# Kernel optimization log

Hardware: AMD Instinct MI355X
Metric: run time of the kernel (lower is better)

Reference implementation:

```python
import jax, jax.numpy as jnp
import numpy as np

B, T, U, V, H = 64, 800, 100, 80, 512
KA, KO = 10, 20
ATT_MULT = 0.05


def setup_inputs() -> dict:
    key = jax.random.key(0)
    ks = jax.random.split(key, 16)
    s = 0.05
    inp = {
        'chars': jax.random.randint(ks[0], (B, U), 0, V, dtype=jnp.int32),
        'chars_mask': jnp.ones((B, U), jnp.float32),
        'strokes': jax.random.normal(ks[1], (B, T, 3), jnp.float32),
        'strokes_mask': jnp.ones((B, T), jnp.float32),
        # lstm_0: LSTMCell(3+V -> H), PyTorch gate order i,f,g,o; biases fused
        'W_ih0': jax.random.normal(ks[2], (4 * H, 3 + V), jnp.float32) * s,
        'W_hh0': jax.random.normal(ks[3], (4 * H, H), jnp.float32) * s,
        'b0': jnp.zeros((4 * H,), jnp.float32),
        # attention linear: H -> 3*KA
        'W_att': jax.random.normal(ks[4], (3 * KA, H), jnp.float32) * s,
        'b_att': jnp.zeros((3 * KA,), jnp.float32),
        # lstm_1: (3+V+H -> H)
        'W_ih1': jax.random.normal(ks[5], (4 * H, 3 + V + H), jnp.float32) * s,
        'W_hh1': jax.random.normal(ks[6], (4 * H, H), jnp.float32) * s,
        'b1': jnp.zeros((4 * H,), jnp.float32),
        # lstm_2: (3+V+H -> H)
        'W_ih2': jax.random.normal(ks[7], (4 * H, 3 + V + H), jnp.float32) * s,
        'W_hh2': jax.random.normal(ks[8], (4 * H, H), jnp.float32) * s,
        'b2': jnp.zeros((4 * H,), jnp.float32),
        # fc: 3H -> 6*KO + 1
        'W_fc': jax.random.normal(ks[9], (6 * KO + 1, 3 * H), jnp.float32) * s,
        'b_fc': jnp.zeros((6 * KO + 1,), jnp.float32),
    }
    return inp


def _lstm_step(h, c, x, W_ih, W_hh, b):
    gates = x @ W_ih.T + h @ W_hh.T + b
    i, f, g, o = jnp.split(gates, 4, axis=-1)
    c = jax.nn.sigmoid(f) * c + jax.nn.sigmoid(i) * jnp.tanh(g)
    h = jax.nn.sigmoid(o) * jnp.tanh(c)
    return h, c


def _lstm_layer(x_btd, W_ih, W_hh, b):
    # x_btd: [B, T, D] -> [B, T, H]
    def step(carry, x_t):
        h, c = carry
        h, c = _lstm_step(h, c, x_t, W_ih, W_hh, b)
        return (h, c), h
    h0 = jnp.zeros((x_btd.shape[0], H), x_btd.dtype)
    c0 = jnp.zeros_like(h0)
    _, hs = jax.lax.scan(step, (h0, c0), jnp.swapaxes(x_btd, 0, 1))
    return jnp.swapaxes(hs, 0, 1)


def _forward(chars, chars_mask, strokes, strokes_mask,
             W_ih0, W_hh0, b0, W_att, b_att,
             W_ih1, W_hh1, b1, W_ih2, W_hh2, b2, W_fc, b_fc):
    ctx = jax.nn.one_hot(chars, V, dtype=jnp.float32) * chars_mask[..., None]  # [B,U,V]
    u = jnp.arange(U, dtype=jnp.float32)  # [U]

    def step(carry, x_t):
        h0, c0, w_t, k_t = carry
        h0, c0 = _lstm_step(h0, c0, jnp.concatenate([x_t, w_t], -1), W_ih0, W_hh0, b0)
        abk = jnp.exp(h0 @ W_att.T + b_att)  # [B, 3*KA]
        alpha, beta, kappa = jnp.split(abk, 3, axis=-1)  # each [B, KA]
        kappa = kappa * ATT_MULT + k_t
        # phi: [B, U]
        phi = jnp.sum(alpha[:, None, :] * jnp.exp(-beta[:, None, :] * (kappa[:, None, :] - u[None, :, None]) ** 2), axis=-1)
        phi = phi * chars_mask
        w_t = jnp.einsum('bu,buv->bv', phi, ctx)
        return (h0, c0, w_t, kappa), (h0, w_t)

    init = (jnp.zeros((B, H)), jnp.zeros((B, H)), jnp.zeros((B, V)), jnp.zeros((B, KA)))
    _, (h0_seq, w_seq) = jax.lax.scan(step, init, jnp.swapaxes(strokes, 0, 1))
    lstm0_out = jnp.swapaxes(h0_seq, 0, 1)      # [B,T,H]
    att_out = jnp.swapaxes(w_seq, 0, 1)         # [B,T,V]

    lstm1_out = _lstm_layer(jnp.concatenate([strokes, att_out, lstm0_out], -1), W_ih1, W_hh1, b1)
    lstm2_out = _lstm_layer(jnp.concatenate([strokes, att_out, lstm1_out], -1), W_ih2, W_hh2, b2)

    last = jnp.concatenate([lstm0_out, lstm1_out, lstm2_out], -1) @ W_fc.T + b_fc  # [B,T,6*KO+1]
    mu, log_sigma, pi, rho, eos = jnp.split(last, [2 * KO, 4 * KO, 5 * KO, 6 * KO], axis=-1)
    rho = jnp.tanh(rho)
    log_pi = jax.nn.log_softmax(pi, axis=-1)
    eos = jax.nn.sigmoid(-eos)
    # packed output: [log_pi | mu | log_sigma | rho | eos] -> [B,T,6*KO+1]
    return jnp.concatenate([log_pi, mu, log_sigma, rho, eos], axis=-1)


def reference(chars, chars_mask, strokes, strokes_mask,
              W_ih0, W_hh0, b0, W_att, b_att,
              W_ih1, W_hh1, b1, W_ih2, W_hh2, b2, W_fc, b_fc):
    return _forward(chars, chars_mask, strokes, strokes_mask,
                    W_ih0, W_hh0, b0, W_att, b_att,
                    W_ih1, W_hh1, b1, W_ih2, W_hh2, b2, W_fc, b_fc)
```

## Files before the change

### kernel.cpp

```cpp
#include <hip/hip_runtime.h>


#define TT   800
#define NOUT 121
#define NEG  (-1073741824)
typedef unsigned long long u64;
typedef unsigned int u32;
typedef __attribute__((ext_vector_type(8))) short short8v;
typedef __attribute__((ext_vector_type(4))) float float4v;

#define RSLOT   65536
#define RWSLOT  12288
#define OFF_SEQ 0
#define OFF_R0  16384
#define OFF_R1  (OFF_R0 + 16 * RSLOT)
#define OFF_R2  (OFF_R1 + 16 * RSLOT)
#define OFF_RW  (OFF_R2 + 16 * RSLOT)
#define OFF_WATT (OFF_RW + 16 * RWSLOT)
#define OFF_OV  (OFF_WATT + 65536)
#define ABLK    36864
#define OFF_WA1 (OFF_OV + 801 * 4096)
#define OFF_WA2 (OFF_WA1 + 256 * ABLK)
#define OFF_WFC (OFF_WA2 + 128 * ABLK)
#define OFF_END (OFF_WFC + 8 * 48 * 1024)

#define MFMA_B16(a, b, c) __builtin_amdgcn_mfma_f32_16x16x32_bf16(a, b, c, 0, 0, 0)

__device__ __forceinline__ float sigmf(float x) { return 1.f / (1.f + __expf(-x)); }
__device__ __forceinline__ float tanhf_(float x) { return 1.f - 2.f / (1.f + __expf(2.f * x)); }
__device__ __forceinline__ unsigned short f2bf(float x) {
    u32 u = __float_as_uint(x);
    return (unsigned short)((u + 0x7FFFu + ((u >> 16) & 1u)) >> 16);
}
__device__ __forceinline__ float bf2f(u32 s) { return __uint_as_float(s << 16); }

__device__ __forceinline__ u64 cl64(const u64* p) {
    return __hip_atomic_load(p, __ATOMIC_RELAXED, __HIP_MEMORY_SCOPE_AGENT);
}
__device__ __forceinline__ u32 cl32(const u32* p) {
    return __hip_atomic_load(p, __ATOMIC_RELAXED, __HIP_MEMORY_SCOPE_AGENT);
}
__device__ __forceinline__ void cs32(u32* p, u32 v) {
    __hip_atomic_store(p, v, __ATOMIC_RELAXED, __HIP_MEMORY_SCOPE_AGENT);
}
__device__ __forceinline__ void cs64(u64* p, u64 v) {
    __hip_atomic_store(p, v, __ATOMIC_RELAXED, __HIP_MEMORY_SCOPE_AGENT);
}

__global__ void prep_zero(u32* ws32) {
    int n = (OFF_WATT - OFF_SEQ) / 4;
    for (int i = blockIdx.x * blockDim.x + threadIdx.x; i < n; i += gridDim.x * blockDim.x) {
        u32 v = 0u;
        if (i < 4096 && (i & 31) == 0) {
            int f = i >> 5;
            if (f >= 104 && f < 128) v = 0x7FFFFFFFu;
        }
        ws32[i] = v;
    }
}
__global__ void prep_ov(const float* __restrict__ strokes, short* __restrict__ dst) {
    int n = 801 * 2048;
    for (int idx = blockIdx.x * blockDim.x + threadIdx.x; idx < n; idx += gridDim.x * blockDim.x) {
        int s = idx >> 11, rem = idx & 2047;
        int t = rem >> 9, lane = (rem >> 3) & 63, j = rem & 7;
        int k = 1088 + (lane >> 4) * 8 + j;
        int b = t * 16 + (lane & 15);
        short v = 0;
        int tt = -1, d = 0;
        if (k >= 1104 && k <= 1106)      { tt = s - 1; d = k - 1104; }
        else if (k >= 1107 && k <= 1109) { tt = s;     d = k - 1107; }
        if (tt >= 0 && tt < TT) v = (short)f2bf(strokes[((size_t)b * TT + tt) * 3 + d]);
        dst[idx] = v;
    }
}
__global__ void prep_watt(const float* __restrict__ W_att, short* __restrict__ dst) {
    int n = 2 * 2 * 16 * 512;
    for (int idx = blockIdx.x * blockDim.x + threadIdx.x; idx < n; idx += gridDim.x * blockDim.x) {
        int part = idx >> 14;
        int mt = (idx >> 13) & 1;
        int c = (idx >> 9) & 15;
        int lane = (idx >> 3) & 63, j = idx & 7;
        int a = mt * 16 + (lane & 15);
        int k = c * 32 + ((lane >> 4) << 3) + j;
        float v = (a < 30) ? W_att[a * 512 + k] : 0.f;
        unsigned short h = f2bf(v);
        if (part) { float r = v - bf2f(h); h = f2bf(r); }
        dst[idx] = (short)h;
    }
}
__global__ void prep_wa1(const float* __restrict__ Wih0, const float* __restrict__ Whh0,
                         const float* __restrict__ Wih1, const float* __restrict__ Whh1,
                         short* __restrict__ dst) {
    int n = 256 * 36 * 512;
    for (int idx = blockIdx.x * blockDim.x + threadIdx.x; idx < n; idx += gridDim.x * blockDim.x) {
        int blk = idx / 18432, rem = idx % 18432;
        int c = rem >> 9, r2 = rem & 511, lane = r2 >> 3, j = r2 & 7;
        int m = lane & 15, q = lane >> 4;
        int k = c * 32 + q * 8 + j;
        int gate = m & 3, hloc = m >> 2;
        float v = 0.f;
        if (blk < 128) {
            int grow = gate * 512 + blk * 4 + hloc;
            if (k >= 512 && k < 1024)       v = Whh0[(size_t)grow * 512 + (k - 512)];
            else if (k >= 1024 && k < 1104) v = Wih0[(size_t)grow * 83 + 3 + (k - 1024)];
            else if (k >= 1107 && k < 1110) v = Wih0[(size_t)grow * 83 + (k - 1107)];
        } else {
            int grow = gate * 512 + (blk - 128) * 4 + hloc;
            if (k < 512)        v = Whh1[(size_t)grow * 512 + k];
            else if (k < 1024)  v = Wih1[(size_t)grow * 595 + 83 + (k - 512)];
            else if (k < 1104)  v = Wih1[(size_t)grow * 595 + 3 + (k - 1024)];
            else if (k < 1107)  v = Wih1[(size_t)grow * 595 + (k - 1104)];
        }
        dst[idx] = (short)f2bf(v);
    }
}
__global__ void prep_wa2(const float* __restrict__ Wih2, const float* __restrict__ Whh2,
                         short* __restrict__ dst) {
    int n = 128 * 36 * 512;
    for (int idx = blockIdx.x * blockDim.x + threadIdx.x; idx < n; idx += gridDim.x * blockDim.x) {
        int blk = idx / 18432, rem = idx % 18432;
        int c = rem >> 9, r2 = rem & 511, lane = r2 >> 3, j = r2 & 7;
        int m = lane & 15, q = lane >> 4;
        int k = c * 32 + q * 8 + j;
        int grow = (m & 3) * 512 + blk * 4 + (m >> 2);
        float v = 0.f;
        if (k < 512)        v = Whh2[(size_t)grow * 512 + k];
        else if (k < 1024)  v = Wih2[(size_t)grow * 595 + 83 + (k - 512)];
        else if (k < 1104)  v = Wih2[(size_t)grow * 595 + 3 + (k - 1024)];
        else if (k < 1107)  v = Wih2[(size_t)grow * 595 + (k - 1104)];
        dst[idx] = (short)f2bf(v);
    }
}
__global__ void prep_wfc(const float* __restrict__ W_fc, short* __restrict__ dst) {
    int n = 8 * 48 * 512;
    for (int idx = blockIdx.x * blockDim.x + threadIdx.x; idx < n; idx += gridDim.x * blockDim.x) {
        int mt = idx / 24576, rem = idx % 24576;
        int c = rem >> 9, r2 = rem & 511, lane = r2 >> 3, j = r2 & 7;
        int o = mt * 16 + (lane & 15);
        int k = c * 32 + (lane >> 4) * 8 + j;
        float v = (o < NOUT) ? W_fc[(size_t)o * 1536 + k] : 0.f;
        dst[idx] = (short)f2bf(v);
    }
}

__device__ __forceinline__ void waitf2(u32* SEQ, int i1, int t1, int i2, int t2, int wv) {
    if (wv == 0) {
        int sl = 0;
        while (1) {
            int v1 = (int)cl32(SEQ + i1 * 32);
            int v2 = (int)cl32(SEQ + i2 * 32);
            if (__all((v1 >= t1) & (v2 >= t2))) break;
            if (sl < 7) ++sl;
            switch (sl) {
                case 3: __builtin_amdgcn_s_sleep(1); break;
                case 4: __builtin_amdgcn_s_sleep(2); break;
                case 5: __builtin_amdgcn_s_sleep(4); break;
                case 6: __builtin_amdgcn_s_sleep(8); break;
                case 7: __builtin_amdgcn_s_sleep(16); break;
                default: break;
            }
        }
    }
    __syncthreads();
}
__device__ __forceinline__ void waitf1(u32* SEQ, int i1, int t1, int wv) {
    if (wv == 0) {
        int sl = 0;
        while (1) {
            int v1 = (int)cl32(SEQ + i1 * 32);
            if (__all(v1 >= t1)) break;
            if (sl < 7) ++sl;
            switch (sl) {
                case 3: __builtin_amdgcn_s_sleep(1); break;
                case 4: __builtin_amdgcn_s_sleep(2); break;
                case 5: __builtin_amdgcn_s_sleep(4); break;
                case 6: __builtin_amdgcn_s_sleep(8); break;
                case 7: __builtin_amdgcn_s_sleep(16); break;
                default: break;
            }
        }
    }
    __syncthreads();
}
__device__ __forceinline__ void publish(u32* SEQ, int idx, int val) {
    asm volatile("s_waitcnt vmcnt(0)" ::: "memory");
    __syncthreads();
    if (threadIdx.x == 0) cs32(SEQ + idx * 32, (u32)val);
}

__device__ __forceinline__ void store_h(char* slot, int nb, int mt, int nt,
                                        int q, int nn, u32 hb) {
    u32 g1 = (u32)__shfl((int)hb, nn + 16, 64);
    u32 g2 = (u32)__shfl((int)hb, nn + 32, 64);
    u32 g3 = (u32)__shfl((int)hb, nn + 48, 64);
    if (q == 0) {
        int k0 = nb * 16 + mt * 4;
        int ck = k0 >> 5, qq = (k0 >> 3) & 3, j0 = k0 & 7;
        u64 pk = (u64)(hb & 0xFFFFu) | ((u64)(g1 & 0xFFFFu) << 16)
               | ((u64)(g2 & 0xFFFFu) << 32) | ((u64)(g3 & 0xFFFFu) << 48);
        u64* dst = (u64*)(slot + ((((ck * 4 + nt) * 64 + qq * 16 + nn) * 8 + j0) * 2));
        cs64(dst, pk);
    }
}

__device__ __forceinline__ float4v gemm_run(const short* __restrict__ Ab,
                                            const short* __restrict__ pB,
                                            int c0, int cN, float4v acc) {
    short8v a0 = *(const short8v*)(Ab + (size_t)(c0 + 0) * 512);
    short8v a1 = *(const short8v*)(Ab + (size_t)(c0 + 1) * 512);
    short8v a2 = *(const short8v*)(Ab + (size_t)(c0 + 2) * 512);
    short8v a3 = *(const short8v*)(Ab + (size_t)(c0 + 3) * 512);
    short8v a4 = *(const short8v*)(Ab + (size_t)(c0 + 4) * 512);
    short8v a5 = *(const short8v*)(Ab + (size_t)(c0 + 5) * 512);
    short8v a6 = *(const short8v*)(Ab + (size_t)(c0 + 6) * 512);
    short8v a7 = *(const short8v*)(Ab + (size_t)(c0 + 7) * 512);
    int c = c0;
    short8v bv;
#pragma unroll 1
    for (; c + 8 < cN; c += 8) {
        bv = *(const short8v*)(pB + (size_t)(c + 0) * 2048);
        acc = MFMA_B16(a0, bv, acc);
        if (c + 8 < cN)  a0 = *(const short8v*)(Ab + (size_t)(c + 8) * 512);
        bv = *(const short8v*)(pB + (size_t)(c + 1) * 2048);
        acc = MFMA_B16(a1, bv, acc);
        if (c + 9 < cN)  a1 = *(const short8v*)(Ab + (size_t)(c + 9) * 512);
        bv = *(const short8v*)(pB + (size_t)(c + 2) * 2048);
        acc = MFMA_B16(a2, bv, acc);
        if (c + 10 < cN) a2 = *(const short8v*)(Ab + (size_t)(c + 10) * 512);
        bv = *(const short8v*)(pB + (size_t)(c + 3) * 2048);
        acc = MFMA_B16(a3, bv, acc);
        if (c + 11 < cN) a3 = *(const short8v*)(Ab + (size_t)(c + 11) * 512);
        bv = *(const short8v*)(pB + (size_t)(c + 4) * 2048);
        acc = MFMA_B16(a4, bv, acc);
        if (c + 12 < cN) a4 = *(const short8v*)(Ab + (size_t)(c + 12) * 512);
        bv = *(const short8v*)(pB + (size_t)(c + 5) * 2048);
        acc = MFMA_B16(a5, bv, acc);
        if (c + 13 < cN) a5 = *(const short8v*)(Ab + (size_t)(c + 13) * 512);
        bv = *(const short8v*)(pB + (size_t)(c + 6) * 2048);
        acc = MFMA_B16(a6, bv, acc);
        if (c + 14 < cN) a6 = *(const short8v*)(Ab + (size_t)(c + 14) * 512);
        bv = *(const short8v*)(pB + (size_t)(c + 7) * 2048);
        acc = MFMA_B16(a7, bv, acc);
        if (c + 15 < cN) a7 = *(const short8v*)(Ab + (size_t)(c + 15) * 512);
    }
    int r = cN - c;
    bv = *(const short8v*)(pB + (size_t)(c + 0) * 2048);
    acc = MFMA_B16(a0, bv, acc);
    if (r > 1) { bv = *(const short8v*)(pB + (size_t)(c + 1) * 2048); acc = MFMA_B16(a1, bv, acc); }
    if (r > 2) { bv = *(const short8v*)(pB + (size_t)(c + 2) * 2048); acc = MFMA_B16(a2, bv, acc); }
    if (r > 3) { bv = *(const short8v*)(pB + (size_t)(c + 3) * 2048); acc = MFMA_B16(a3, bv, acc); }
    if (r > 4) { bv = *(const short8v*)(pB + (size_t)(c + 4) * 2048); acc = MFMA_B16(a4, bv, acc); }
    if (r > 5) { bv = *(const short8v*)(pB + (size_t)(c + 5) * 2048); acc = MFMA_B16(a5, bv, acc); }
    if (r > 6) { bv = *(const short8v*)(pB + (size_t)(c + 6) * 2048); acc = MFMA_B16(a6, bv, acc); }
    if (r > 7) { bv = *(const short8v*)(pB + (size_t)(c + 7) * 2048); acc = MFMA_B16(a7, bv, acc); }
    return acc;
}

__global__ void __launch_bounds__(1024, 4)
hand_pipeline(const int* __restrict__ chars, const float* __restrict__ chars_mask,
              const float* __restrict__ b_att,
              const float* __restrict__ b0, const float* __restrict__ b1,
              const float* __restrict__ b2, const float* __restrict__ b_fc,
              float* ws, float* __restrict__ out) {
    __shared__ short panel[36 * 4 * 64 * 8];
    char* wsB = (char*)ws;
    u32* SEQ = (u32*)(wsB + OFF_SEQ);
    u64* pan8 = (u64*)panel;
    const int tid = threadIdx.x;
    const int blk = blockIdx.x;
    const int lid = tid & 63;
    const int wv  = __builtin_amdgcn_readfirstlane(tid >> 6);
    const int q   = lid >> 4, nn = lid & 15;
    const int mt  = wv >> 2, nt = wv & 3;
    const int role = blk >> 5;
    const int nb   = blk & 31;

    float* ABK  = (float*)panel;
    float* KAP  = ABK + 2048;
    float* WCTX = KAP + 640;
    unsigned char* CH8 = (unsigned char*)(WCTX + 5184);
    float* M2   = (float*)(CH8 + 6400);
    float* BATT = M2 + 6400;

    for (int i = tid; i < 18432; i += 1024) pan8[i] = 0ull;
    __syncthreads();

    float biasr[4] = {0.f, 0.f, 0.f, 0.f};
    if (role < 3) {
        const float* bp = role == 0 ? b0 : role == 1 ? b1 : b2;
        int hg = nb * 16 + mt * 4 + q;
#pragma unroll
        for (int r = 0; r < 4; ++r) biasr[r] = bp[r * 512 + hg];
    }
    if (role == 0) {
        for (int i = tid; i < 6400; i += 1024) {
            int u2 = i >> 6, b = i & 63;
            CH8[i] = (unsigned char)chars[b * 100 + u2];
            float m = chars_mask[b * 100 + u2];
            M2[i] = m * m;
        }
        if (tid < 640) KAP[tid] = 0.f;
        if (tid < 32) BATT[tid] = (tid < 30) ? b_att[tid] : 0.f;
    }
    __syncthreads();

    const short* WA1 = (const short*)(wsB + OFF_WA1);
    const short* WA2 = (const short*)(wsB + OFF_WA2);
    float cst = 0.f;

    if (role == 0) {
        const short* Ab = WA1 + (size_t)(nb * 4 + mt) * 18432 + lid * 8;
        const short* pB = panel + (size_t)(nt * 64 + lid) * 8;
        for (int s = 0; s <= TT; ++s) {
            if ((s & 7) == 0) waitf2(SEQ, 32 + lid, s - 8, 96 + (lid & 7), s - 8, wv);
            {
                const u64* sO = (const u64*)(wsB + OFF_OV + (size_t)s * 4096);
                if (tid < 512) pan8[17408 + tid] = sO[tid];
#pragma unroll
                for (int it = 0; it < 6; ++it) {
                    int i = tid + it * 1024;
                    if (i < 5184) WCTX[i] = 0.f;
                }
            }
            waitf1(SEQ, lid & 31, s, wv);
            {
                const u64* sB = (const u64*)(wsB + OFF_R0 + (size_t)((s - 1) & 15) * RSLOT);
                u64 tb[8];
#pragma unroll
                for (int it = 0; it < 8; ++it) tb[it] = cl64(sB + tid + it * 1024);
#pragma unroll
                for (int it = 0; it < 8; ++it) pan8[8192 + tid + it * 1024] = tb[it];
            }
            __syncthreads();
            const bool actA = (s >= 1);
            float4v acc = {0.f, 0.f, 0.f, 0.f};
            if (wv >= 8) {
                if (s < TT) acc = gemm_run(Ab, pB, 16, 32, acc);
            } else if (actA) {
                const int mta = mt & 1;
                const short* Ah = (const short*)(wsB + OFF_WATT) + (size_t)mta * 8192 + lid * 8;
                const short* Al = Ah + 16384;
                const short* pBA = panel + (size_t)((64 + nt) * 64 + lid) * 8;
                float4v aacc = {0.f, 0.f, 0.f, 0.f};
#pragma unroll 4
                for (int c = 0; c < 16; ++c) {
                    short8v bv = *(const short8v*)(pBA + (size_t)c * 2048);
                    aacc = MFMA_B16(*(const short8v*)(Ah + (size_t)c * 512), bv, aacc);
                    aacc = MFMA_B16(*(const short8v*)(Al + (size_t)c * 512), bv, aacc);
                }
#pragma unroll
                for (int r = 0; r < 4; ++r) {
                    int a = mta * 16 + q * 4 + r;
                    if (a < 30) ABK[a * 64 + nt * 16 + nn] = __expf(aacc[r] + BATT[a]);
                }
            }
            __syncthreads();
            if (actA) {
                const int b = tid & 63;
                float al[10], be[10], kp[10];
#pragma unroll
                for (int ka = 0; ka < 10; ++ka) {
                    al[ka] = ABK[ka * 64 + b];
                    be[ka] = ABK[(10 + ka) * 64 + b];
                    kp[ka] = KAP[ka * 64 + b] + 0.05f * ABK[(20 + ka) * 64 + b];
                }
                for (int i = tid; i < 6400; i += 1024) {
                    float fu = (float)(i >> 6);
                    float ph = 0.f;
#pragma unroll
                    for (int ka = 0; ka < 10; ++ka) {
                        float d = kp[ka] - fu;
                        ph = fmaf(al[ka], __expf(-be[ka] * d * d), ph);
                    }
                    float m2 = M2[i];
                    if (m2 != 0.f) atomicAdd(&WCTX[b * 81 + CH8[i]], ph * m2);
                }
            }
            __syncthreads();
            if (wv < 8) {
                if (s < TT) acc = gemm_run(Ab, pB, 16, 32, acc);
            } else if (actA) {
                const int st = tid - 512;
#pragma unroll
                for (int ii = 0; ii < 2; ++ii) {
                    int i = st + ii * 512;
                    if (i < 640) KAP[i] += 0.05f * ABK[(20 + (i >> 6)) * 64 + (i & 63)];
                }
                for (int idx = st; idx < 6144; idx += 512) {
                    int c = idx >> 11, rem = idx & 2047;
                    int nt2 = rem >> 9, l = (rem >> 3) & 63, j = rem & 7;
                    int k = 1024 + c * 32 + ((l >> 4) << 3) + j;
                    if (k < 1104) {
                        int b = nt2 * 16 + (l & 15);
                        panel[(size_t)(((32 + c) * 4 + nt2) * 64 + l) * 8 + j] =
                            (short)f2bf(WCTX[b * 81 + (k - 1024)]);
                    }
                }
                if (st < 80) {
                    int bsel = st / 40, p = st - bsel * 40;
                    int bb = nb * 2 + bsel;
                    int k = 1024 + p * 2;
                    int lc = (k - 1024) >> 5, qq = (k >> 3) & 3, j = k & 7;
                    char* slot = wsB + OFF_RW + (size_t)((s - 1) & 15) * RWSLOT;
                    u32* dst = (u32*)(slot +
                        ((((lc * 4 + (bb >> 4)) * 64 + qq * 16 + (bb & 15)) * 8 + j) * 2));
                    cs32(dst, (u32)f2bf(WCTX[bb * 81 + 2 * p]) |
                              ((u32)f2bf(WCTX[bb * 81 + 2 * p + 1]) << 16));
                }
            }
            __syncthreads();
            if (s < TT) {
#pragma unroll
                for (int c = 32; c < 35; ++c) {
                    short8v av = *(const short8v*)(Ab + (size_t)c * 512);
                    short8v bv = *(const short8v*)(pB + (size_t)c * 2048);
                    acc = MFMA_B16(av, bv, acc);
                }
                float gi = acc[0] + biasr[0], gf = acc[1] + biasr[1];
                float gg = acc[2] + biasr[2], go = acc[3] + biasr[3];
                cst = sigmf(gf) * cst + sigmf(gi) * tanhf_(gg);
                float h = sigmf(go) * tanhf_(cst);
                store_h(wsB + OFF_R0 + (size_t)(s & 15) * RSLOT, nb, mt, nt, q, nn, f2bf(h));
            }
            publish(SEQ, blk, s + 1);
        }
    } else if (role < 3) {
        const short* Ab = (role == 1 ? WA1 + (size_t)(128 + nb * 4 + mt) * 18432
                                     : WA2 + (size_t)(nb * 4 + mt) * 18432) + lid * 8;
        const short* pB = panel + (size_t)(nt * 64 + lid) * 8;
        for (int t = 0; t < TT; ++t) {
            if ((t & 7) == 0) {
                if (role == 1) waitf2(SEQ, 64 + (lid & 31), t - 8, 96 + (lid & 7), t - 8, wv);
                else           waitf1(SEQ, 96 + (lid & 7), t - 8, wv);
            }
            if (role == 1) waitf1(SEQ, 32 + (lid & 31), t, wv);
            else           waitf1(SEQ, 64 + (lid & 31), t, wv);
            const u64* sA = (const u64*)(wsB + (role == 1 ? OFF_R1 : OFF_R2) +
                                         (size_t)((t - 1) & 15) * RSLOT);
            u64 ta[8];
#pragma unroll
            for (int it = 0; it < 8; ++it) ta[it] = cl64(sA + tid + it * 1024);
            if (role == 1) waitf1(SEQ, lid & 31, t + 2, wv);
            else           waitf1(SEQ, lid, (lid < 32) ? t + 2 : t + 1, wv);
            {
                const u64* sB = (role == 1)
                    ? (const u64*)(wsB + OFF_R0 + (size_t)(t & 15) * RSLOT)
                    : (const u64*)(wsB + OFF_R1 + (size_t)(t & 15) * RSLOT);
                const u64* sW = (const u64*)(wsB + OFF_RW + (size_t)(t & 15) * RWSLOT);
                const u64* sO = (const u64*)(wsB + OFF_OV + (size_t)(t + 1) * 4096);
                u64 tb[8];
#pragma unroll
                for (int it = 0; it < 8; ++it) tb[it] = cl64(sB + tid + it * 1024);
                u64 tw = cl64(sW + tid);
                u64 tov = (tid < 512) ? (cl64(sW + 1024 + tid) | sO[tid]) : 0ull;
#pragma unroll
                for (int it = 0; it < 8; ++it) pan8[tid + it * 1024] = ta[it];
#pragma unroll
                for (int it = 0; it < 8; ++it) pan8[8192 + tid + it * 1024] = tb[it];
                pan8[16384 + tid] = tw;
                if (tid < 512) pan8[17408 + tid] = tov;
            }
            __syncthreads();
            {
                float4v acc = {0.f, 0.f, 0.f, 0.f};
                acc = gemm_run(Ab, pB, 0, 35, acc);
                float gi = acc[0] + biasr[0], gf = acc[1] + biasr[1];
                float gg = acc[2] + biasr[2], go = acc[3] + biasr[3];
                cst = sigmf(gf) * cst + sigmf(gi) * tanhf_(gg);
                float h = sigmf(go) * tanhf_(cst);
                store_h(wsB + (role == 1 ? OFF_R1 : OFF_R2) + (size_t)(t & 15) * RSLOT,
                        nb, mt, nt, q, nn, f2bf(h));
            }
            publish(SEQ, blk, t + 1);
        }
    } else {
        const int fcb = blk - 96;
        const int kq = wv >> 2, ntw = wv & 3;
        float* FR = (float*)panel;
        for (int t = 0; t < TT; ++t) {
            waitf2(SEQ, lid, t + 1, 64 + (lid & 31), t + 1, wv);
            const char* p0 = wsB + OFF_R0 + (size_t)(t & 15) * RSLOT;
            const char* p1 = wsB + OFF_R1 + (size_t)(t & 15) * RSLOT;
            const char* p2 = wsB + OFF_R2 + (size_t)(t & 15) * RSLOT;
            const int boff = ntw * 1024 + lid * 16;
            auto BLD = [&](int C) -> short8v {
                const char* p = (C < 16) ? p0 + (size_t)C * 4096
                             : (C < 32) ? p1 + (size_t)(C - 16) * 4096
                                        : p2 + (size_t)(C - 32) * 4096;
                const u64* q8 = (const u64*)(p + boff);
                union { u64 w[2]; short8v v; } uu;
                uu.w[0] = cl64(q8); uu.w[1] = cl64(q8 + 1);
                return uu.v;
            };
            const short* Ab = (const short*)(wsB + OFF_WFC) + (size_t)fcb * 24576 + lid * 8;
            const int cb = kq * 12;
            short8v bvv[12];
#pragma unroll
            for (int i = 0; i < 12; ++i) bvv[i] = BLD(cb + i);
            short8v av[6];
#pragma unroll
            for (int i = 0; i < 6; ++i)
                av[i] = *(const short8v*)(Ab + (size_t)(cb + i) * 512);
            float4v acc = {0.f, 0.f, 0.f, 0.f};
#pragma unroll
            for (int i = 0; i < 6; ++i) {
                acc = MFMA_B16(av[i], bvv[i], acc);
                av[i] = *(const short8v*)(Ab + (size_t)(cb + 6 + i) * 512);
            }
#pragma unroll
            for (int i = 0; i < 6; ++i) acc = MFMA_B16(av[i], bvv[6 + i], acc);
#pragma unroll
            for (int r = 0; r < 4; ++r) FR[(wv * 64 + lid) * 4 + r] = acc[r];
            __syncthreads();
            if (kq == 0) {
#pragma unroll
                for (int r = 0; r < 4; ++r)
                    acc[r] = FR[(wv * 64 + lid) * 4 + r] + FR[((wv + 4) * 64 + lid) * 4 + r]
                           + FR[((wv + 8) * 64 + lid) * 4 + r] + FR[((wv + 12) * 64 + lid) * 4 + r];
                const int bb = ntw * 16 + nn;
                float* po = out + ((size_t)bb * TT + t) * NOUT + fcb * 16 + q * 4;
#pragma unroll
                for (int r = 0; r < 4; ++r) {
                    int o = fcb * 16 + q * 4 + r;
                    if (o < NOUT) po[r] = acc[r] + b_fc[o];
                }
            }
            publish(SEQ, blk, t + 1);
        }
    }
}

__global__ void postproc_kernel(float* __restrict__ out) {
    int row  = blockIdx.x * 8 + (threadIdx.x >> 5);
    int lane = threadIdx.x & 31;
    float* r = out + (size_t)row * NOUT;
    float pv = (lane < 20) ? r[80 + lane] : -1e30f;
    float m = pv;
#pragma unroll
    for (int off = 16; off; off >>= 1) m = fmaxf(m, __shfl_xor(m, off, 32));
    float e = (lane < 20) ? __expf(pv - m) : 0.f;
    float sm = e;
#pragma unroll
    for (int off = 16; off; off >>= 1) sm += __shfl_xor(sm, off, 32);
    float logZ = m + __logf(sm);
    float res[4];
    bool wr[4];
    int ps[4];
#pragma unroll
    for (int i = 0; i < 4; ++i) {
        int p = lane + 32 * i;
        ps[i] = p;
        wr[i] = (p < NOUT);
        float x = 0.f;
        if (p < 20)       x = pv - logZ;
        else if (p < 100) { if (wr[i]) x = r[p - 20]; }
        else if (p < 120) x = tanhf_(r[p]);
        else if (p == 120) x = 1.f / (1.f + __expf(r[120]));
        res[i] = x;
    }
#pragma unroll
    for (int i = 0; i < 4; ++i)
        if (wr[i]) r[ps[i]] = res[i];
}

extern "C" void kernel_launch(void* const* d_in, const int* in_sizes, int n_in,
                              void* d_out, int out_size, void* d_ws, size_t ws_size,
                              hipStream_t stream) {
    const int*   chars      = (const int*)d_in[0];
    const float* chars_mask = (const float*)d_in[1];
    const float* strokes    = (const float*)d_in[2];
    const float* W_ih0 = (const float*)d_in[4];
    const float* W_hh0 = (const float*)d_in[5];
    const float* b0    = (const float*)d_in[6];
    const float* W_att = (const float*)d_in[7];
    const float* b_att = (const float*)d_in[8];
    const float* W_ih1 = (const float*)d_in[9];
    const float* W_hh1 = (const float*)d_in[10];
    const float* b1    = (const float*)d_in[11];
    const float* W_ih2 = (const float*)d_in[12];
    const float* W_hh2 = (const float*)d_in[13];
    const float* b2    = (const float*)d_in[14];
    const float* W_fc  = (const float*)d_in[15];
    const float* b_fc  = (const float*)d_in[16];
    float* ws  = (float*)d_ws;
    float* out = (float*)d_out;
    char*  wsB = (char*)d_ws;

    prep_zero<<<512, 256, 0, stream>>>((u32*)ws);
    prep_ov<<<1024, 256, 0, stream>>>(strokes, (short*)(wsB + OFF_OV));
    prep_watt<<<64, 256, 0, stream>>>(W_att, (short*)(wsB + OFF_WATT));
    prep_wa1<<<2048, 256, 0, stream>>>(W_ih0, W_hh0, W_ih1, W_hh1, (short*)(wsB + OFF_WA1));
    prep_wa2<<<1024, 256, 0, stream>>>(W_ih2, W_hh2, (short*)(wsB + OFF_WA2));
    prep_wfc<<<256, 256, 0, stream>>>(W_fc, (short*)(wsB + OFF_WFC));

    hand_pipeline<<<104, 1024, 0, stream>>>(chars, chars_mask, b_att,
                                            b0, b1, b2, b_fc, ws, out);
    postproc_kernel<<<(64 * TT) / 8, 256, 0, stream>>>(out);
}
```

Measured before the change: 15.82 ms.

## Halve LSTM workgroup count by giving each wave two batch tiles

```diff
diff --git a/kernel.cpp b/kernel.cpp
--- a/kernel.cpp
+++ b/kernel.cpp
@@ -53,7 +53,7 @@
         u32 v = 0u;
         if (i < 4096 && (i & 31) == 0) {
             int f = i >> 5;
-            if (f >= 104 && f < 128) v = 0x7FFFFFFFu;
+            if (f >= 56 && f < 128) v = 0x7FFFFFFFu;
         }
         ws32[i] = v;
     }
@@ -188,13 +188,12 @@
     if (threadIdx.x == 0) cs32(SEQ + idx * 32, (u32)val);
 }
 
-__device__ __forceinline__ void store_h(char* slot, int nb, int mt, int nt,
+__device__ __forceinline__ void store_h(char* slot, int k0, int nt,
                                         int q, int nn, u32 hb) {
     u32 g1 = (u32)__shfl((int)hb, nn + 16, 64);
     u32 g2 = (u32)__shfl((int)hb, nn + 32, 64);
     u32 g3 = (u32)__shfl((int)hb, nn + 48, 64);
     if (q == 0) {
-        int k0 = nb * 16 + mt * 4;
         int ck = k0 >> 5, qq = (k0 >> 3) & 3, j0 = k0 & 7;
         u64 pk = (u64)(hb & 0xFFFFu) | ((u64)(g1 & 0xFFFFu) << 16)
                | ((u64)(g2 & 0xFFFFu) << 32) | ((u64)(g3 & 0xFFFFu) << 48);
@@ -203,57 +202,47 @@
     }
 }
 
-__device__ __forceinline__ float4v gemm_run(const short* __restrict__ Ab,
-                                            const short* __restrict__ pB,
-                                            int c0, int cN, float4v acc) {
+__device__ __forceinline__ void gemm_run2(const short* __restrict__ Ab,
+                                          const short* __restrict__ pB0,
+                                          const short* __restrict__ pB1,
+                                          int c0, int cN,
+                                          float4v& acc0, float4v& acc1) {
     short8v a0 = *(const short8v*)(Ab + (size_t)(c0 + 0) * 512);
     short8v a1 = *(const short8v*)(Ab + (size_t)(c0 + 1) * 512);
     short8v a2 = *(const short8v*)(Ab + (size_t)(c0 + 2) * 512);
     short8v a3 = *(const short8v*)(Ab + (size_t)(c0 + 3) * 512);
-    short8v a4 = *(const short8v*)(Ab + (size_t)(c0 + 4) * 512);
-    short8v a5 = *(const short8v*)(Ab + (size_t)(c0 + 5) * 512);
-    short8v a6 = *(const short8v*)(Ab + (size_t)(c0 + 6) * 512);
-    short8v a7 = *(const short8v*)(Ab + (size_t)(c0 + 7) * 512);
     int c = c0;
     short8v bv;
 #pragma unroll 1
-    for (; c + 8 < cN; c += 8) {
-        bv = *(const short8v*)(pB + (size_t)(c + 0) * 2048);
-        acc = MFMA_B16(a0, bv, acc);
-        if (c + 8 < cN)  a0 = *(const short8v*)(Ab + (size_t)(c + 8) * 512);
-        bv = *(const short8v*)(pB + (size_t)(c + 1) * 2048);
-        acc = MFMA_B16(a1, bv, acc);
-        if (c + 9 < cN)  a1 = *(const short8v*)(Ab + (size_t)(c + 9) * 512);
-        bv = *(const short8v*)(pB + (size_t)(c + 2) * 2048);
-        acc = MFMA_B16(a2, bv, acc);
-        if (c + 10 < cN) a2 = *(const short8v*)(Ab + (size_t)(c + 10) * 512);
-        bv = *(const short8v*)(pB + (size_t)(c + 3) * 2048);
-        acc = MFMA_B16(a3, bv, acc);
-        if (c + 11 < cN) a3 = *(const short8v*)(Ab + (size_t)(c + 11) * 512);
-        bv = *(const short8v*)(pB + (size_t)(c + 4) * 2048);
-        acc = MFMA_B16(a4, bv, acc);
-        if (c + 12 < cN) a4 = *(const short8v*)(Ab + (size_t)(c + 12) * 512);
-        bv = *(const short8v*)(pB + (size_t)(c + 5) * 2048);
-        acc = MFMA_B16(a5, bv, acc);
-        if (c + 13 < cN) a5 = *(const short8v*)(Ab + (size_t)(c + 13) * 512);
-        bv = *(const short8v*)(pB + (size_t)(c + 6) * 2048);
-        acc = MFMA_B16(a6, bv, acc);
-        if (c + 14 < cN) a6 = *(const short8v*)(Ab + (size_t)(c + 14) * 512);
-        bv = *(const short8v*)(pB + (size_t)(c + 7) * 2048);
-        acc = MFMA_B16(a7, bv, acc);
-        if (c + 15 < cN) a7 = *(const short8v*)(Ab + (size_t)(c + 15) * 512);
+    for (; c + 4 < cN; c += 4) {
+        bv = *(const short8v*)(pB0 + (size_t)(c + 0) * 2048); acc0 = MFMA_B16(a0, bv, acc0);
+        bv = *(const short8v*)(pB1 + (size_t)(c + 0) * 2048); acc1 = MFMA_B16(a0, bv, acc1);
+        if (c + 4 < cN) a0 = *(const short8v*)(Ab + (size_t)(c + 4) * 512);
+        bv = *(const short8v*)(pB0 + (size_t)(c + 1) * 2048); acc0 = MFMA_B16(a1, bv, acc0);
+        bv = *(const short8v*)(pB1 + (size_t)(c + 1) * 2048); acc1 = MFMA_B16(a1, bv, acc1);
+        if (c + 5 < cN) a1 = *(const short8v*)(Ab + (size_t)(c + 5) * 512);
+        bv = *(const short8v*)(pB0 + (size_t)(c + 2) * 2048); acc0 = MFMA_B16(a2, bv, acc0);
+        bv = *(const short8v*)(pB1 + (size_t)(c + 2) * 2048); acc1 = MFMA_B16(a2, bv, acc1);
+        if (c + 6 < cN) a2 = *(const short8v*)(Ab + (size_t)(c + 6) * 512);
+        bv = *(const short8v*)(pB0 + (size_t)(c + 3) * 2048); acc0 = MFMA_B16(a3, bv, acc0);
+        bv = *(const short8v*)(pB1 + (size_t)(c + 3) * 2048); acc1 = MFMA_B16(a3, bv, acc1);
+        if (c + 7 < cN) a3 = *(const short8v*)(Ab + (size_t)(c + 7) * 512);
     }
     int r = cN - c;
-    bv = *(const short8v*)(pB + (size_t)(c + 0) * 2048);
-    acc = MFMA_B16(a0, bv, acc);
-    if (r > 1) { bv = *(const short8v*)(pB + (size_t)(c + 1) * 2048); acc = MFMA_B16(a1, bv, acc); }
-    if (r > 2) { bv = *(const short8v*)(pB + (size_t)(c + 2) * 2048); acc = MFMA_B16(a2, bv, acc); }
-    if (r > 3) { bv = *(const short8v*)(pB + (size_t)(c + 3) * 2048); acc = MFMA_B16(a3, bv, acc); }
-    if (r > 4) { bv = *(const short8v*)(pB + (size_t)(c + 4) * 2048); acc = MFMA_B16(a4, bv, acc); }
-    if (r > 5) { bv = *(const short8v*)(pB + (size_t)(c + 5) * 2048); acc = MFMA_B16(a5, bv, acc); }
-    if (r > 6) { bv = *(const short8v*)(pB + (size_t)(c + 6) * 2048); acc = MFMA_B16(a6, bv, acc); }
-    if (r > 7) { bv = *(const short8v*)(pB + (size_t)(c + 7) * 2048); acc = MFMA_B16(a7, bv, acc); }
-    return acc;
+    bv = *(const short8v*)(pB0 + (size_t)(c + 0) * 2048); acc0 = MFMA_B16(a0, bv, acc0);
+    bv = *(const short8v*)(pB1 + (size_t)(c + 0) * 2048); acc1 = MFMA_B16(a0, bv, acc1);
+    if (r > 1) {
+        bv = *(const short8v*)(pB0 + (size_t)(c + 1) * 2048); acc0 = MFMA_B16(a1, bv, acc0);
+        bv = *(const short8v*)(pB1 + (size_t)(c + 1) * 2048); acc1 = MFMA_B16(a1, bv, acc1);
+    }
+    if (r > 2) {
+        bv = *(const short8v*)(pB0 + (size_t)(c + 2) * 2048); acc0 = MFMA_B16(a2, bv, acc0);
+        bv = *(const short8v*)(pB1 + (size_t)(c + 2) * 2048); acc1 = MFMA_B16(a2, bv, acc1);
+    }
+    if (r > 3) {
+        bv = *(const short8v*)(pB0 + (size_t)(c + 3) * 2048); acc0 = MFMA_B16(a3, bv, acc0);
+        bv = *(const short8v*)(pB1 + (size_t)(c + 3) * 2048); acc1 = MFMA_B16(a3, bv, acc1);
+    }
 }
 
 __global__ void __launch_bounds__(1024, 4)
@@ -271,9 +260,10 @@
     const int lid = tid & 63;
     const int wv  = __builtin_amdgcn_readfirstlane(tid >> 6);
     const int q   = lid >> 4, nn = lid & 15;
-    const int mt  = wv >> 2, nt = wv & 3;
-    const int role = blk >> 5;
-    const int nb   = blk & 31;
+    const int mt  = wv >> 1, ntp = wv & 1;
+    const int nt0 = ntp * 2, nt1 = ntp * 2 + 1;
+    const int role = blk >> 4;
+    const int nb   = blk & 15;
 
     float* ABK  = (float*)panel;
     float* KAP  = ABK + 2048;
@@ -288,7 +278,7 @@
     float biasr[4] = {0.f, 0.f, 0.f, 0.f};
     if (role < 3) {
         const float* bp = role == 0 ? b0 : role == 1 ? b1 : b2;
-        int hg = nb * 16 + mt * 4 + q;
+        int hg = nb * 32 + mt * 4 + q;
 #pragma unroll
         for (int r = 0; r < 4; ++r) biasr[r] = bp[r * 512 + hg];
     }
@@ -306,13 +296,16 @@
 
     const short* WA1 = (const short*)(wsB + OFF_WA1);
     const short* WA2 = (const short*)(wsB + OFF_WA2);
-    float cst = 0.f;
+    float cst0 = 0.f, cst1 = 0.f;
 
     if (role == 0) {
-        const short* Ab = WA1 + (size_t)(nb * 4 + mt) * 18432 + lid * 8;
-        const short* pB = panel + (size_t)(nt * 64 + lid) * 8;
+        const short* Ab = WA1 + (size_t)(nb * 8 + mt) * 18432 + lid * 8;
+        const short* pB0 = panel + (size_t)(nt0 * 64 + lid) * 8;
+        const short* pB1 = panel + (size_t)(nt1 * 64 + lid) * 8;
+        const int mta = (wv >> 2) & 1, nta = wv & 3;
+        const short* pBA = panel + (size_t)((64 + nta) * 64 + lid) * 8;
         for (int s = 0; s <= TT; ++s) {
-            if ((s & 7) == 0) waitf2(SEQ, 32 + lid, s - 8, 96 + (lid & 7), s - 8, wv);
+            if ((s & 7) == 0) waitf2(SEQ, 16 + (lid & 31), s - 8, 48 + (lid & 7), s - 8, wv);
             {
                 const u64* sO = (const u64*)(wsB + OFF_OV + (size_t)s * 4096);
                 if (tid < 512) pan8[17408 + tid] = sO[tid];
@@ -322,7 +315,7 @@
                     if (i < 5184) WCTX[i] = 0.f;
                 }
             }
-            waitf1(SEQ, lid & 31, s, wv);
+            waitf1(SEQ, lid & 15, s, wv);
             {
                 const u64* sB = (const u64*)(wsB + OFF_R0 + (size_t)((s - 1) & 15) * RSLOT);
                 u64 tb[8];
@@ -333,14 +326,13 @@
             }
             __syncthreads();
             const bool actA = (s >= 1);
-            float4v acc = {0.f, 0.f, 0.f, 0.f};
+            float4v acc0 = {0.f, 0.f, 0.f, 0.f};
+            float4v acc1 = {0.f, 0.f, 0.f, 0.f};
             if (wv >= 8) {
-                if (s < TT) acc = gemm_run(Ab, pB, 16, 32, acc);
+                if (s < TT) gemm_run2(Ab, pB0, pB1, 16, 32, acc0, acc1);
             } else if (actA) {
-                const int mta = mt & 1;
                 const short* Ah = (const short*)(wsB + OFF_WATT) + (size_t)mta * 8192 + lid * 8;
                 const short* Al = Ah + 16384;
-                const short* pBA = panel + (size_t)((64 + nt) * 64 + lid) * 8;
                 float4v aacc = {0.f, 0.f, 0.f, 0.f};
 #pragma unroll 4
                 for (int c = 0; c < 16; ++c) {
@@ -351,7 +343,7 @@
 #pragma unroll
                 for (int r = 0; r < 4; ++r) {
                     int a = mta * 16 + q * 4 + r;
-                    if (a < 30) ABK[a * 64 + nt * 16 + nn] = __expf(aacc[r] + BATT[a]);
+                    if (a < 30) ABK[a * 64 + nta * 16 + nn] = __expf(aacc[r] + BATT[a]);
                 }
             }
             __syncthreads();
@@ -378,7 +370,7 @@
             }
             __syncthreads();
             if (wv < 8) {
-                if (s < TT) acc = gemm_run(Ab, pB, 16, 32, acc);
+                if (s < TT) gemm_run2(Ab, pB0, pB1, 16, 32, acc0, acc1);
             } else if (actA) {
                 const int st = tid - 512;
 #pragma unroll
@@ -396,9 +388,9 @@
                             (short)f2bf(WCTX[b * 81 + (k - 1024)]);
                     }
                 }
-                if (st < 80) {
+                if (st < 160) {
                     int bsel = st / 40, p = st - bsel * 40;
-                    int bb = nb * 2 + bsel;
+                    int bb = nb * 4 + bsel;
                     int k = 1024 + p * 2;
                     int lc = (k - 1024) >> 5, qq = (k >> 3) & 3, j = k & 7;
                     char* slot = wsB + OFF_RW + (size_t)((s - 1) & 15) * RWSLOT;
@@ -413,35 +405,50 @@
 #pragma unroll
                 for (int c = 32; c < 35; ++c) {
                     short8v av = *(const short8v*)(Ab + (size_t)c * 512);
-                    short8v bv = *(const short8v*)(pB + (size_t)c * 2048);
-                    acc = MFMA_B16(av, bv, acc);
-                }
-                float gi = acc[0] + biasr[0], gf = acc[1] + biasr[1];
-                float gg = acc[2] + biasr[2], go = acc[3] + biasr[3];
-                cst = sigmf(gf) * cst + sigmf(gi) * tanhf_(gg);
-                float h = sigmf(go) * tanhf_(cst);
-                store_h(wsB + OFF_R0 + (size_t)(s & 15) * RSLOT, nb, mt, nt, q, nn, f2bf(h));
+                    short8v bv0 = *(const short8v*)(pB0 + (size_t)c * 2048);
+                    acc0 = MFMA_B16(av, bv0, acc0);
+                    short8v bv1 = *(const short8v*)(pB1 + (size_t)c * 2048);
+                    acc1 = MFMA_B16(av, bv1, acc1);
+                }
+                char* slot = wsB + OFF_R0 + (size_t)(s & 15) * RSLOT;
+                const int k0 = nb * 32 + mt * 4;
+                {
+                    float gi = acc0[0] + biasr[0], gf = acc0[1] + biasr[1];
+                    float gg = acc0[2] + biasr[2], go = acc0[3] + biasr[3];
+                    cst0 = sigmf(gf) * cst0 + sigmf(gi) * tanhf_(gg);
+                    float h = sigmf(go) * tanhf_(cst0);
+                    store_h(slot, k0, nt0, q, nn, f2bf(h));
+                }
+                {
+                    float gi = acc1[0] + biasr[0], gf = acc1[1] + biasr[1];
+                    float gg = acc1[2] + biasr[2], go = acc1[3] + biasr[3];
+                    cst1 = sigmf(gf) * cst1 + sigmf(gi) * tanhf_(gg);
+                    float h = sigmf(go) * tanhf_(cst1);
+                    store_h(slot, k0, nt1, q, nn, f2bf(h));
+                }
             }
             publish(SEQ, blk, s + 1);
         }
     } else if (role < 3) {
-        const short* Ab = (role == 1 ? WA1 + (size_t)(128 + nb * 4 + mt) * 18432
-                                     : WA2 + (size_t)(nb * 4 + mt) * 18432) + lid * 8;
-        const short* pB = panel + (size_t)(nt * 64 + lid) * 8;
+        const short* Ab = (role == 1 ? WA1 + (size_t)(128 + nb * 8 + mt) * 18432
+                                     : WA2 + (size_t)(nb * 8 + mt) * 18432) + lid * 8;
+        const short* pB0 = panel + (size_t)(nt0 * 64 + lid) * 8;
+        const short* pB1 = panel + (size_t)(nt1 * 64 + lid) * 8;
         for (int t = 0; t < TT; ++t) {
             if ((t & 7) == 0) {
-                if (role == 1) waitf2(SEQ, 64 + (lid & 31), t - 8, 96 + (lid & 7), t - 8, wv);
-                else           waitf1(SEQ, 96 + (lid & 7), t - 8, wv);
-            }
-            if (role == 1) waitf1(SEQ, 32 + (lid & 31), t, wv);
-            else           waitf1(SEQ, 64 + (lid & 31), t, wv);
+                if (role == 1) waitf2(SEQ, 32 + (lid & 15), t - 8, 48 + (lid & 7), t - 8, wv);
+                else           waitf1(SEQ, 48 + (lid & 7), t - 8, wv);
+            }
+            if (role == 1) waitf1(SEQ, 16 + (lid & 15), t, wv);
+            else           waitf1(SEQ, 32 + (lid & 15), t, wv);
             const u64* sA = (const u64*)(wsB + (role == 1 ? OFF_R1 : OFF_R2) +
                                          (size_t)((t - 1) & 15) * RSLOT);
             u64 ta[8];
 #pragma unroll
             for (int it = 0; it < 8; ++it) ta[it] = cl64(sA + tid + it * 1024);
-            if (role == 1) waitf1(SEQ, lid & 31, t + 2, wv);
-            else           waitf1(SEQ, lid, (lid < 32) ? t + 2 : t + 1, wv);
+            if (role == 1) waitf1(SEQ, lid & 15, t + 2, wv);
+            else           waitf1(SEQ, (lid < 32) ? (lid & 15) : 16 + (lid & 15),
+                                  (lid < 32) ? t + 2 : t + 1, wv);
             {
                 const u64* sB = (role == 1)
                     ? (const u64*)(wsB + OFF_R0 + (size_t)(t & 15) * RSLOT)
@@ -462,23 +469,34 @@
             }
             __syncthreads();
             {
-                float4v acc = {0.f, 0.f, 0.f, 0.f};
-                acc = gemm_run(Ab, pB, 0, 35, acc);
-                float gi = acc[0] + biasr[0], gf = acc[1] + biasr[1];
-                float gg = acc[2] + biasr[2], go = acc[3] + biasr[3];
-                cst = sigmf(gf) * cst + sigmf(gi) * tanhf_(gg);
-                float h = sigmf(go) * tanhf_(cst);
-                store_h(wsB + (role == 1 ? OFF_R1 : OFF_R2) + (size_t)(t & 15) * RSLOT,
-                        nb, mt, nt, q, nn, f2bf(h));
+                float4v acc0 = {0.f, 0.f, 0.f, 0.f};
+                float4v acc1 = {0.f, 0.f, 0.f, 0.f};
+                gemm_run2(Ab, pB0, pB1, 0, 35, acc0, acc1);
+                char* slot = wsB + (role == 1 ? OFF_R1 : OFF_R2) + (size_t)(t & 15) * RSLOT;
+                const int k0 = nb * 32 + mt * 4;
+                {
+                    float gi = acc0[0] + biasr[0], gf = acc0[1] + biasr[1];
+                    float gg = acc0[2] + biasr[2], go = acc0[3] + biasr[3];
+                    cst0 = sigmf(gf) * cst0 + sigmf(gi) * tanhf_(gg);
+                    float h = sigmf(go) * tanhf_(cst0);
+                    store_h(slot, k0, nt0, q, nn, f2bf(h));
+                }
+                {
+                    float gi = acc1[0] + biasr[0], gf = acc1[1] + biasr[1];
+                    float gg = acc1[2] + biasr[2], go = acc1[3] + biasr[3];
+                    cst1 = sigmf(gf) * cst1 + sigmf(gi) * tanhf_(gg);
+                    float h = sigmf(go) * tanhf_(cst1);
+                    store_h(slot, k0, nt1, q, nn, f2bf(h));
+                }
             }
             publish(SEQ, blk, t + 1);
         }
     } else {
-        const int fcb = blk - 96;
+        const int fcb = blk - 48;
         const int kq = wv >> 2, ntw = wv & 3;
         float* FR = (float*)panel;
         for (int t = 0; t < TT; ++t) {
-            waitf2(SEQ, lid, t + 1, 64 + (lid & 31), t + 1, wv);
+            waitf2(SEQ, lid & 15, t + 1, 16 + (lid & 31), t + 1, wv);
             const char* p0 = wsB + OFF_R0 + (size_t)(t & 15) * RSLOT;
             const char* p1 = wsB + OFF_R1 + (size_t)(t & 15) * RSLOT;
             const char* p2 = wsB + OFF_R2 + (size_t)(t & 15) * RSLOT;
@@ -593,7 +611,7 @@
     prep_wa2<<<1024, 256, 0, stream>>>(W_ih2, W_hh2, (short*)(wsB + OFF_WA2));
     prep_wfc<<<256, 256, 0, stream>>>(W_fc, (short*)(wsB + OFF_WFC));
 
-    hand_pipeline<<<104, 1024, 0, stream>>>(chars, chars_mask, b_att,
-                                            b0, b1, b2, b_fc, ws, out);
+    hand_pipeline<<<56, 1024, 0, stream>>>(chars, chars_mask, b_att,
+                                           b0, b1, b2, b_fc, ws, out);
     postproc_kernel<<<(64 * TT) / 8, 256, 0, stream>>>(out);
 }
```

Result: faster. 15.13 ms (-4.4%).
